# Kernel optimization log

Hardware: AMD Instinct MI355X
Metric: run time of the kernel (lower is better)

The kernel has to match this reference:

```python
import jax, jax.numpy as jnp
import numpy as np


def setup_inputs() -> dict:
    key = jax.random.key(0)
    k1, k2 = jax.random.split(key, 2)
    N, H, W, FIN = 64, 64, 64, 64
    FH, FW, FOUT = 4, 4, 128
    L = (H // FH) * (W // FW)  # 256 output locations (stride == kernel)
    X = jax.random.normal(k1, (N, H, W, FIN), dtype=jnp.float32)
    # 'alexnet' init: normal(0, 0.01), unshared per-location filters
    filters = 0.01 * jax.random.normal(k2, (1, L, FH, FW, FIN, FOUT), dtype=jnp.float32)
    bias = jnp.zeros((FOUT,), dtype=jnp.float32)  # bias init value 0.0
    return {"X": X, "filters": filters, "bias": bias}


def reference(X, filters, bias):
    N, H, W, C = X.shape
    _, L, fh, fw, fin, fout = filters.shape
    rows, cols = H // fh, W // fw
    # image_to_patches (stride==kernel branch): non-overlapping patch extraction
    # patches[n, r*cols+c, i, j, ch] = X[n, r*fh+i, c*fw+j, ch]
    patches = X.reshape(N, rows, fh, cols, fw, C)
    patches = patches.transpose(0, 1, 3, 2, 4, 5).reshape(N, L, fh, fw, C)
    # broadcast-multiply + reduce_sum over (fh, fw, fin) == per-location GEMM
    Z = jnp.einsum('nlijc,lijcf->nlf', patches, filters[0]) + bias
    Z = Z.reshape(N, rows, cols, fout)
    return jax.nn.relu(Z)
```

## Files before the change

kernel.cpp:

```cpp
#include <hip/hip_runtime.h>


typedef __bf16 bf16x8 __attribute__((ext_vector_type(8)));
typedef float f32x4 __attribute__((ext_vector_type(4)));

#define SBQ 36

__device__ __forceinline__ unsigned pack2(float a, float b) {
  __bf16 lo = (__bf16)a, hi = (__bf16)b;
  return (unsigned)__builtin_bit_cast(unsigned short, lo) |
         ((unsigned)__builtin_bit_cast(unsigned short, hi) << 16);
}
__device__ __forceinline__ bf16x8 cvt8(float4 lo, float4 hi) {
  uint4 v;
  v.x = pack2(lo.x, lo.y);
  v.y = pack2(lo.z, lo.w);
  v.z = pack2(hi.x, hi.y);
  v.w = pack2(hi.z, hi.w);
  return __builtin_bit_cast(bf16x8, v);
}

__global__ __launch_bounds__(256, 4) void bioconv_wave4(
    const float* __restrict__ X, const float* __restrict__ Fw,
    const float* __restrict__ bias, float* __restrict__ out) {
  const int bx = blockIdx.x;
  const int xcd = bx & 7;
  const int idx = bx >> 3;
  const int l = xcd * 32 + (idx >> 2);
  const int fq = idx & 3;
  const int r = l >> 4, c = l & 15;
  const int tid = threadIdx.x;
  const int wave = tid >> 6;
  const int lane = tid & 63;
  const int q = lane >> 4, nl = lane & 15;

  __shared__ __align__(16) unsigned Bs[4][2][16 * SBQ];

  const float* pA =
      X + (size_t)(wave * 16 + nl) * 262144 + r * 16384 + c * 256 + q * 8;

  const float* pB = Fw + (size_t)l * 131072 + fq * 32 + (lane >> 3) * 256 + (lane & 7) * 4;
  unsigned* const wpB = (unsigned*)Bs[wave] + ((lane >> 3) * SBQ + (lane & 7) * 4);

  float4 aR[2][2];
  float4 bR[3][4];
  f32x4 acc[2];
  acc[0] = (f32x4){0.f, 0.f, 0.f, 0.f};
  acc[1] = (f32x4){0.f, 0.f, 0.f, 0.f};

  auto issueA = [&](int s, int ring) {
    const int p = s >> 1;
    const int off = (p >> 2) * 4096 + (p & 3) * 64 + (s & 1) * 32;
    aR[ring][0] = *(const float4*)(pA + off);
    aR[ring][1] = *(const float4*)(pA + off + 4);
  };
  auto issueB = [&](int s, int ring) {
#pragma unroll
    for (int rep = 0; rep < 2; ++rep) {
      const float* g = pB + s * 4096 + rep * 2048;
      bR[ring][rep * 2] = *(const float4*)(g);
      bR[ring][rep * 2 + 1] = *(const float4*)(g + 128);
    }
  };
  auto writeB = [&](int s, int ring) {
    unsigned* wp = wpB + (s & 1) * (16 * SBQ);
#pragma unroll
    for (int rep = 0; rep < 2; ++rep) {
      float4 e0 = bR[ring][rep * 2], e1 = bR[ring][rep * 2 + 1];
      uint4 v;
      v.x = pack2(e0.x, e1.x);
      v.y = pack2(e0.y, e1.y);
      v.z = pack2(e0.z, e1.z);
      v.w = pack2(e0.w, e1.w);
      *(uint4*)(wp + rep * 8 * SBQ) = v;
    }
  };

  issueA(0, 0);
  issueB(0, 0);
  issueA(1, 1);
  issueB(1, 1);
  issueB(2, 2);
  writeB(0, 0);

#pragma unroll
  for (int s = 0; s < 32; ++s) {
    if (s + 3 < 32) issueB(s + 3, (s + 3) % 3);
    if (s + 1 < 32) writeB(s + 1, (s + 1) % 3);

    bf16x8 af = cvt8(aR[s & 1][0], aR[s & 1][1]);
    if (s + 2 < 32) issueA(s + 2, s & 1);

#pragma unroll
    for (int fb = 0; fb < 2; ++fb) {
      const unsigned* bp = &Bs[wave][s & 1][(q * 4) * SBQ + fb * 16 + nl];
      uint4 v;
      v.x = bp[0];
      v.y = bp[SBQ];
      v.z = bp[2 * SBQ];
      v.w = bp[3 * SBQ];
      bf16x8 bfr = __builtin_bit_cast(bf16x8, v);
      acc[fb] = __builtin_amdgcn_mfma_f32_16x16x32_bf16(af, bfr, acc[fb], 0, 0, 0);
    }
  }

#pragma unroll
  for (int fb = 0; fb < 2; ++fb) {
    const int f = fq * 32 + fb * 16 + nl;
    const float bv = bias[f];
    float* ob = out + (size_t)l * 128 + f;
#pragma unroll
    for (int v = 0; v < 4; ++v) {
      const int row = wave * 16 + q * 4 + v;
      ob[(size_t)row * 32768] = fmaxf(acc[fb][v] + bv, 0.f);
    }
  }
}

extern "C" void kernel_launch(void* const* d_in, const int* in_sizes, int n_in,
                              void* d_out, int out_size, void* d_ws, size_t ws_size,
                              hipStream_t stream) {
  const float* X = (const float*)d_in[0];
  const float* Fw = (const float*)d_in[1];
  const float* bias = (const float*)d_in[2];
  float* out = (float*)d_out;
  bioconv_wave4<<<1024, 256, 0, stream>>>(X, Fw, bias, out);
}
```

Baseline: 252.3 us.

## Stage input patches and filters in LDS, shared across a 512-thread block

The kernel now uses 512-thread blocks that each compute 64 output channels for one location, instead of 256-thread blocks computing 32. Both the input patch tile and the filter tile are converted to bf16 and double-buffered in shared memory, with an XOR swizzle on the activation tile. All eight waves read the shared activation tile, so X is fetched half as many times from global memory and the main loop runs 8 stages of depth 128 instead of 32 stages. The cost is a block-wide barrier every stage, about 67KB of LDS per block that limits blocks per CU, and shallower register prefetch.

```diff
diff --git a/kernel.cpp b/kernel.cpp
--- a/kernel.cpp
+++ b/kernel.cpp
@@ -4,114 +4,130 @@
 typedef __bf16 bf16x8 __attribute__((ext_vector_type(8)));
 typedef float f32x4 __attribute__((ext_vector_type(4)));
 
-#define SBQ 36
-
 __device__ __forceinline__ unsigned pack2(float a, float b) {
   __bf16 lo = (__bf16)a, hi = (__bf16)b;
   return (unsigned)__builtin_bit_cast(unsigned short, lo) |
          ((unsigned)__builtin_bit_cast(unsigned short, hi) << 16);
 }
-__device__ __forceinline__ bf16x8 cvt8(float4 lo, float4 hi) {
-  uint4 v;
-  v.x = pack2(lo.x, lo.y);
-  v.y = pack2(lo.z, lo.w);
-  v.z = pack2(hi.x, hi.y);
-  v.w = pack2(hi.z, hi.w);
-  return __builtin_bit_cast(bf16x8, v);
-}
 
-__global__ __launch_bounds__(256, 4) void bioconv_wave4(
+__global__ __launch_bounds__(512, 4) void bioconv_blk(
     const float* __restrict__ X, const float* __restrict__ Fw,
     const float* __restrict__ bias, float* __restrict__ out) {
   const int bx = blockIdx.x;
   const int xcd = bx & 7;
   const int idx = bx >> 3;
-  const int l = xcd * 32 + (idx >> 2);
-  const int fq = idx & 3;
+  const int l = xcd * 32 + (idx >> 1);
+  const int fh = idx & 1;
   const int r = l >> 4, c = l & 15;
-  const int tid = threadIdx.x;
-  const int wave = tid >> 6;
-  const int lane = tid & 63;
+
+  const int t = threadIdx.x;
+  const int wave = t >> 6, lane = t & 63;
   const int q = lane >> 4, nl = lane & 15;
+  const int m0 = (wave >> 1) * 16;
+  const int n0 = (wave & 1) * 32;
 
-  __shared__ __align__(16) unsigned Bs[4][2][16 * SBQ];
+  __shared__ __align__(16) unsigned short As[2][64 * 128];
+  __shared__ __align__(16) unsigned Bs[2][64 * 68];
 
-  const float* pA =
-      X + (size_t)(wave * 16 + nl) * 262144 + r * 16384 + c * 256 + q * 8;
+  const int arow = t >> 3;
+  const int alane = t & 7;
+  const float* gA = X + (size_t)arow * 262144 + r * 16384 + c * 256;
+  const float* gB = Fw + (size_t)l * 131072 + fh * 64 + (size_t)arow * 256;
 
-  const float* pB = Fw + (size_t)l * 131072 + fq * 32 + (lane >> 3) * 256 + (lane & 7) * 4;
-  unsigned* const wpB = (unsigned*)Bs[wave] + ((lane >> 3) * SBQ + (lane & 7) * 4);
+  float4 vA[4], vB[4];
 
-  float4 aR[2][2];
-  float4 bR[3][4];
+  auto loadA = [&](int s) {
+    const float* g = gA + (s >> 1) * 4096 + (s & 1) * 128;
+#pragma unroll
+    for (int rep = 0; rep < 4; ++rep)
+      vA[rep] = *(const float4*)(g + (alane + rep * 8) * 4);
+  };
+  auto loadB = [&](int s) {
+    const float* g = gB + s * 16384;
+#pragma unroll
+    for (int rep = 0; rep < 2; ++rep) {
+      vB[rep * 2] = *(const float4*)(g + (alane + rep * 8) * 4);
+      vB[rep * 2 + 1] = *(const float4*)(g + 128 + (alane + rep * 8) * 4);
+    }
+  };
+  auto writeA = [&](int buf) {
+    unsigned* base = (unsigned*)&As[buf][0];
+#pragma unroll
+    for (int rep = 0; rep < 4; ++rep) {
+      const int f4 = alane + rep * 8;
+      uint2 u;
+      u.x = pack2(vA[rep].x, vA[rep].y);
+      u.y = pack2(vA[rep].z, vA[rep].w);
+      *(uint2*)(base + arow * 64 + ((f4 * 2) ^ ((arow & 7) << 2))) = u;
+    }
+  };
+  auto writeB = [&](int buf) {
+    unsigned* base = (unsigned*)&Bs[buf][0];
+#pragma unroll
+    for (int rep = 0; rep < 2; ++rep) {
+      const int f4 = alane + rep * 8;
+      uint4 v;
+      v.x = pack2(vB[rep * 2].x, vB[rep * 2 + 1].x);
+      v.y = pack2(vB[rep * 2].y, vB[rep * 2 + 1].y);
+      v.z = pack2(vB[rep * 2].z, vB[rep * 2 + 1].z);
+      v.w = pack2(vB[rep * 2].w, vB[rep * 2 + 1].w);
+      *(uint4*)(base + arow * 68 + f4 * 4) = v;
+    }
+  };
+
   f32x4 acc[2];
   acc[0] = (f32x4){0.f, 0.f, 0.f, 0.f};
   acc[1] = (f32x4){0.f, 0.f, 0.f, 0.f};
 
-  auto issueA = [&](int s, int ring) {
-    const int p = s >> 1;
-    const int off = (p >> 2) * 4096 + (p & 3) * 64 + (s & 1) * 32;
-    aR[ring][0] = *(const float4*)(pA + off);
-    aR[ring][1] = *(const float4*)(pA + off + 4);
-  };
-  auto issueB = [&](int s, int ring) {
+  auto compute = [&](int buf) {
 #pragma unroll
-    for (int rep = 0; rep < 2; ++rep) {
-      const float* g = pB + s * 4096 + rep * 2048;
-      bR[ring][rep * 2] = *(const float4*)(g);
-      bR[ring][rep * 2 + 1] = *(const float4*)(g + 128);
-    }
-  };
-  auto writeB = [&](int s, int ring) {
-    unsigned* wp = wpB + (s & 1) * (16 * SBQ);
+    for (int kk = 0; kk < 4; ++kk) {
+      const unsigned short* ap =
+          &As[buf][(m0 + nl) * 128 + ((kk * 32 + q * 8) ^ ((nl & 7) << 3))];
+      bf16x8 af = *(const bf16x8*)ap;
 #pragma unroll
-    for (int rep = 0; rep < 2; ++rep) {
-      float4 e0 = bR[ring][rep * 2], e1 = bR[ring][rep * 2 + 1];
-      uint4 v;
-      v.x = pack2(e0.x, e1.x);
-      v.y = pack2(e0.y, e1.y);
-      v.z = pack2(e0.z, e1.z);
-      v.w = pack2(e0.w, e1.w);
-      *(uint4*)(wp + rep * 8 * SBQ) = v;
+      for (int fb = 0; fb < 2; ++fb) {
+        const unsigned* bp =
+            (const unsigned*)&Bs[buf][0] + (kk * 16 + q * 4) * 68 + n0 + fb * 16 + nl;
+        uint4 v;
+        v.x = bp[0];
+        v.y = bp[68];
+        v.z = bp[136];
+        v.w = bp[204];
+        bf16x8 bfr = __builtin_bit_cast(bf16x8, v);
+        acc[fb] = __builtin_amdgcn_mfma_f32_16x16x32_bf16(af, bfr, acc[fb], 0, 0, 0);
+      }
     }
   };
 
-  issueA(0, 0);
-  issueB(0, 0);
-  issueA(1, 1);
-  issueB(1, 1);
-  issueB(2, 2);
-  writeB(0, 0);
-
+  loadA(0);
+  loadB(0);
+  writeA(0);
+  writeB(0);
+  loadA(1);
+  loadB(1);
 #pragma unroll
-  for (int s = 0; s < 32; ++s) {
-    if (s + 3 < 32) issueB(s + 3, (s + 3) % 3);
-    if (s + 1 < 32) writeB(s + 1, (s + 1) % 3);
-
-    bf16x8 af = cvt8(aR[s & 1][0], aR[s & 1][1]);
-    if (s + 2 < 32) issueA(s + 2, s & 1);
-
-#pragma unroll
-    for (int fb = 0; fb < 2; ++fb) {
-      const unsigned* bp = &Bs[wave][s & 1][(q * 4) * SBQ + fb * 16 + nl];
-      uint4 v;
-      v.x = bp[0];
-      v.y = bp[SBQ];
-      v.z = bp[2 * SBQ];
-      v.w = bp[3 * SBQ];
-      bf16x8 bfr = __builtin_bit_cast(bf16x8, v);
-      acc[fb] = __builtin_amdgcn_mfma_f32_16x16x32_bf16(af, bfr, acc[fb], 0, 0, 0);
+  for (int s = 0; s < 8; ++s) {
+    __syncthreads();
+    compute(s & 1);
+    if (s + 1 < 8) {
+      writeA((s + 1) & 1);
+      writeB((s + 1) & 1);
+    }
+    if (s + 2 < 8) {
+      loadA(s + 2);
+      loadB(s + 2);
     }
   }
 
 #pragma unroll
   for (int fb = 0; fb < 2; ++fb) {
-    const int f = fq * 32 + fb * 16 + nl;
+    const int f = fh * 64 + n0 + fb * 16 + nl;
     const float bv = bias[f];
     float* ob = out + (size_t)l * 128 + f;
 #pragma unroll
     for (int v = 0; v < 4; ++v) {
-      const int row = wave * 16 + q * 4 + v;
+      const int row = m0 + q * 4 + v;
       ob[(size_t)row * 32768] = fmaxf(acc[fb][v] + bv, 0.f);
     }
   }
@@ -124,5 +140,5 @@
   const float* Fw = (const float*)d_in[1];
   const float* bias = (const float*)d_in[2];
   float* out = (float*)d_out;
-  bioconv_wave4<<<1024, 256, 0, stream>>>(X, Fw, bias, out);
+  bioconv_blk<<<512, 512, 0, stream>>>(X, Fw, bias, out);
 }
```

Result: faster. 238.9 us (-5.3%).
